# Performance work log

Hardware: AMD Instinct MI355X
Metric: run time of the kernel (lower is better)

## Reference

```python
import jax, jax.numpy as jnp
import numpy as np

B, C, H, W = 64, 512, 64, 64
RED = 16
HID = C // RED  # 32
N_EXPERTS = 3

def setup_inputs() -> dict:
    key = jax.random.key(0)
    k1, k2, k3, k4 = jax.random.split(key, 4)
    x = jax.random.normal(k1, (B, C, H, W), dtype=jnp.float32)
    dataset = jax.random.randint(k2, (B,), 0, N_EXPERTS, dtype=jnp.int32)
    # torch Linear weight layout: [out_features, in_features]
    W1 = jax.random.normal(k3, (N_EXPERTS, HID, C), dtype=jnp.float32) * (1.0 / np.sqrt(C))
    W2 = jax.random.normal(k4, (N_EXPERTS, C, HID), dtype=jnp.float32) * (1.0 / np.sqrt(HID))
    return {"x": x, "dataset": dataset, "W1": W1, "W2": W2}

def reference(x, dataset, W1, W2):
    # global average pool: [B, C]
    y = jnp.mean(x, axis=(2, 3))
    # per-sample expert weights, routed by dataset id
    w1 = W1[dataset]  # [B, HID, C]
    w2 = W2[dataset]  # [B, C, HID]
    h = jax.nn.relu(jnp.einsum('bc,bhc->bh', y, w1))
    gate = jax.nn.sigmoid(jnp.einsum('bh,bch->bc', h, w2))  # [B, C]
    return x * gate[:, :, None, None]
```

## Files before the change

### kernel.cpp

```cpp
#include <hip/hip_runtime.h>
#include <math.h>

#define NB 64
#define NC 512
#define NHW 4096
#define NHID 32
#define NPLANES (NB * NC)

typedef float f32x4 __attribute__((ext_vector_type(4)));

__global__ __launch_bounds__(256) void pool_kernel(const float* __restrict__ x,
                                                   float* __restrict__ y) {
    const int wid   = threadIdx.x >> 6;
    const int lane  = threadIdx.x & 63;
    const int plane = blockIdx.x * 4 + wid;
    const f32x4* __restrict__ xin =
        reinterpret_cast<const f32x4*>(x + (size_t)plane * NHW);

    float s = 0.f;
#pragma unroll
    for (int i = 0; i < 16; ++i) {
        f32x4 v = xin[lane + i * 64];
        s += v.x + v.y + v.z + v.w;
    }
#pragma unroll
    for (int o = 32; o; o >>= 1) s += __shfl_down(s, o, 64);
    if (lane == 0) y[plane] = s * (1.0f / NHW);
}

__global__ __launch_bounds__(256) void gate_kernel(const float* __restrict__ y,
                                                   const int* __restrict__ dataset,
                                                   const float* __restrict__ W1,
                                                   const float* __restrict__ W2,
                                                   float* __restrict__ gate) {
    const int b = blockIdx.x;
    const int tid = threadIdx.x;

    __shared__ float ys[NC];
    __shared__ float hs[NHID];

    ys[tid]       = y[b * NC + tid];
    ys[tid + 256] = y[b * NC + tid + 256];
    const int e = dataset[b];
    __syncthreads();

    const int hid = tid >> 3;
    const int j   = tid & 7;
    const float* __restrict__ w1row = W1 + ((size_t)e * NHID + hid) * NC;
    float acc = 0.f;
    for (int c = j; c < NC; c += 8) acc += ys[c] * w1row[c];
#pragma unroll
    for (int o = 4; o; o >>= 1) acc += __shfl_down(acc, o, 8);
    if (j == 0) hs[hid] = fmaxf(acc, 0.f);
    __syncthreads();

    const float* __restrict__ w2base = W2 + (size_t)e * NC * NHID;
#pragma unroll
    for (int k = 0; k < 2; ++k) {
        const int c = tid + k * 256;
        const float* __restrict__ w2row = w2base + c * NHID;
        float z = 0.f;
#pragma unroll
        for (int hh = 0; hh < NHID; ++hh) z += hs[hh] * w2row[hh];
        gate[b * NC + c] = 1.0f / (1.0f + expf(-z));
    }
}

__global__ __launch_bounds__(256) void scale_kernel(const float* __restrict__ x,
                                                    const float* __restrict__ gate,
                                                    float* __restrict__ out) {
    const int pair = blockIdx.x;
    const int p0 = pair * 2;
    const float g0 = gate[p0];
    const float g1 = gate[p0 + 1];
    const size_t base = (size_t)pair * 2048;
    const f32x4* __restrict__ xin = reinterpret_cast<const f32x4*>(x);
    f32x4* __restrict__ o4 = reinterpret_cast<f32x4*>(out);
    const int t = threadIdx.x;

#pragma unroll
    for (int k = 0; k < 4; ++k) {
        const size_t i = base + (size_t)k * 256 + t;
        f32x4 v = xin[i];
        v *= g0;
        o4[i] = v;
    }
#pragma unroll
    for (int k = 0; k < 4; ++k) {
        const size_t i = base + 1024 + (size_t)k * 256 + t;
        f32x4 v = xin[i];
        v *= g1;
        o4[i] = v;
    }
}

extern "C" void kernel_launch(void* const* d_in, const int* in_sizes, int n_in,
                              void* d_out, int out_size, void* d_ws, size_t ws_size,
                              hipStream_t stream) {
    const float* x       = (const float*)d_in[0];
    const int*   dataset = (const int*)d_in[1];
    const float* W1      = (const float*)d_in[2];
    const float* W2      = (const float*)d_in[3];
    float* out = (float*)d_out;

    float* y    = (float*)d_ws;
    float* gate = y + NB * NC;

    pool_kernel<<<NPLANES / 4, 256, 0, stream>>>(x, y);
    gate_kernel<<<NB, 256, 0, stream>>>(y, dataset, W1, W2, gate);
    scale_kernel<<<NPLANES / 2, 256, 0, stream>>>(x, gate, out);
}
```

Measured before the change: 325.8 us.

## Reverse scale block order, batch 16 loads per thread, use nontemporal stores

The scale kernel now handles four planes per block and visits blocks in reverse order, so the planes the pool kernel read last, which may still sit in the last-level cache, are reread first. Each thread issues all 16 vector loads before doing any multiply, raising memory-level parallelism, and writes the output with nontemporal stores so the output does not evict cached input. The cost is more registers per thread and half as many blocks.

After: 289.1 us. -11.3%, faster.

```diff
diff --git a/kernel.cpp b/kernel.cpp
--- a/kernel.cpp
+++ b/kernel.cpp
@@ -69,29 +69,31 @@
 __global__ __launch_bounds__(256) void scale_kernel(const float* __restrict__ x,
                                                     const float* __restrict__ gate,
                                                     float* __restrict__ out) {
-    const int pair = blockIdx.x;
-    const int p0 = pair * 2;
-    const float g0 = gate[p0];
-    const float g1 = gate[p0 + 1];
-    const size_t base = (size_t)pair * 2048;
+    const int blk = gridDim.x - 1 - blockIdx.x;
+    const int p0 = blk * 4;
+    const size_t base = (size_t)blk * 4096;
     const f32x4* __restrict__ xin = reinterpret_cast<const f32x4*>(x);
     f32x4* __restrict__ o4 = reinterpret_cast<f32x4*>(out);
     const int t = threadIdx.x;
 
+    float g[4];
 #pragma unroll
-    for (int k = 0; k < 4; ++k) {
-        const size_t i = base + (size_t)k * 256 + t;
-        f32x4 v = xin[i];
-        v *= g0;
-        o4[i] = v;
-    }
+    for (int q = 0; q < 4; ++q) g[q] = gate[p0 + q];
+
+    f32x4 v[16];
 #pragma unroll
-    for (int k = 0; k < 4; ++k) {
-        const size_t i = base + 1024 + (size_t)k * 256 + t;
-        f32x4 v = xin[i];
-        v *= g1;
-        o4[i] = v;
-    }
+    for (int q = 0; q < 4; ++q)
+#pragma unroll
+        for (int k = 0; k < 4; ++k)
+            v[q * 4 + k] = xin[base + (size_t)q * 1024 + k * 256 + t];
+
+#pragma unroll
+    for (int q = 0; q < 4; ++q)
+#pragma unroll
+        for (int k = 0; k < 4; ++k) {
+            f32x4 w = v[q * 4 + k] * g[q];
+            __builtin_nontemporal_store(w, &o4[base + (size_t)q * 1024 + k * 256 + t]);
+        }
 }
 
 extern "C" void kernel_launch(void* const* d_in, const int* in_sizes, int n_in,
@@ -108,5 +110,5 @@
 
     pool_kernel<<<NPLANES / 4, 256, 0, stream>>>(x, y);
     gate_kernel<<<NB, 256, 0, stream>>>(y, dataset, W1, W2, gate);
-    scale_kernel<<<NPLANES / 2, 256, 0, stream>>>(x, gate, out);
+    scale_kernel<<<NPLANES / 4, 256, 0, stream>>>(x, gate, out);
 }
```
